# Performance work log

Hardware: AMD Instinct MI355X
Metric: run time of the kernel (lower is better)

Reference implementation:

```python
import jax, jax.numpy as jnp
import numpy as np

TOP_K = 2
N_EXPERTS = 64
NEG_INF = -1e30  # stand-in for -inf; only used implicitly via sparse softmax


def setup_inputs() -> dict:
    key = jax.random.key(0)
    k1, k2, k3, k4 = jax.random.split(key, 4)
    n_embd, n_exp = 2048, N_EXPERTS
    B, S = 4, 4096
    scale = 1.0 / np.sqrt(n_embd)
    return {
        "x": jax.random.normal(k1, (B, S, n_embd), dtype=jnp.float32),
        "noise_eps": jax.random.normal(k2, (B, S, n_exp), dtype=jnp.float32),
        "W_route": jax.random.normal(k3, (n_embd, n_exp), dtype=jnp.float32) * scale,
        "b_route": jnp.zeros((n_exp,), dtype=jnp.float32),
        "W_noise": jax.random.normal(k4, (n_embd, n_exp), dtype=jnp.float32) * scale,
        "b_noise": jnp.zeros((n_exp,), dtype=jnp.float32),
    }


def reference(x, noise_eps, W_route, b_route, W_noise, b_noise):
    # r_act, noise_scale: [B, S, E]
    r_act = jnp.einsum("bsd,de->bse", x, W_route) + b_route
    noise_raw = jnp.einsum("bsd,de->bse", x, W_noise) + b_noise
    noisy = r_act + noise_eps * jax.nn.softplus(noise_raw)

    topk_logits, idx = jax.lax.top_k(noisy, TOP_K)  # [B, S, k]
    # softmax over a -inf-filled scatter == softmax over the top-k values,
    # scattered back with zeros elsewhere (exp(-inf) = 0)
    probs_k = jax.nn.softmax(topk_logits, axis=-1)  # [B, S, k]
    one_hot = jax.nn.one_hot(idx, N_EXPERTS, dtype=probs_k.dtype)  # [B, S, k, E]
    r_out = jnp.einsum("bsk,bske->bse", probs_k, one_hot)
    return r_out, idx
```

## Files before the change

### kernel.cpp

```cpp
#include <hip/hip_runtime.h>
#include <math.h>


typedef _Float16 f16;
typedef _Float16 f16x8 __attribute__((ext_vector_type(8)));
typedef float    f32x4 __attribute__((ext_vector_type(4)));

#define NEMBD 2048
#define NEXP  64
#define TOKB  32
#define PSTR  36
#define PSLC  (128 * PSTR)
#define WSCALE 64.0f
#define INV_WSCALE 0.015625f

union F4H8 { float4 f; f16x8 h; };

__device__ __forceinline__ f16x8 ld16h(const f16* p) {
    F4H8 u; u.f = *(const float4*)p; return u.h;
}

__global__ __launch_bounds__(256) void build_wt(
    const float* __restrict__ Wr, const float* __restrict__ Wn,
    f16* __restrict__ wt_hi, f16* __restrict__ wt_lo)
{
    __shared__ float ws[32][129];
    const int c = blockIdx.x, t = threadIdx.x;
    const int k0 = c * 32;
    {
        const int k  = t >> 3;
        const int n8 = (t & 7) << 3;
        const float* s0 = Wr + (size_t)(k0 + k) * NEXP + n8;
        const float* s1 = Wn + (size_t)(k0 + k) * NEXP + n8;
        #pragma unroll
        for (int j = 0; j < 8; ++j) ws[k][n8 + j] = s0[j];
        #pragma unroll
        for (int j = 0; j < 8; ++j) ws[k][64 + n8 + j] = s1[j];
    }
    __syncthreads();
    {
        const int n  = t >> 1;
        const int kh = (t & 1) << 4;
        f16x8 hv0, hv1, lv0, lv1;
        #pragma unroll
        for (int j = 0; j < 8; ++j) {
            const float v = ws[kh + j][n] * WSCALE;
            const f16 h = (f16)v;
            hv0[j] = h; lv0[j] = (f16)(v - (float)h);
        }
        #pragma unroll
        for (int j = 0; j < 8; ++j) {
            const float v = ws[kh + 8 + j][n] * WSCALE;
            const f16 h = (f16)v;
            hv1[j] = h; lv1[j] = (f16)(v - (float)h);
        }
        const size_t base = ((size_t)c * 128 + n) * 32 + kh;
        *(f16x8*)(wt_hi + base)     = hv0;
        *(f16x8*)(wt_hi + base + 8) = hv1;
        *(f16x8*)(wt_lo + base)     = lv0;
        *(f16x8*)(wt_lo + base + 8) = lv1;
    }
}

__global__ __launch_bounds__(512, 4) void router_fused6(
    const float* __restrict__ x, const float* __restrict__ eps,
    const f16* __restrict__ wt_hi, const f16* __restrict__ wt_lo,
    const float* __restrict__ br, const float* __restrict__ bn,
    float* __restrict__ out_r, float* __restrict__ out_idx)
{
    __shared__ __align__(16) float P[4 * PSLC];
    __shared__ float TK[4 * TOKB];

    const int tid  = threadIdx.x;
    const int lane = tid & 63;
    const int w    = tid >> 6;
    const int m0   = blockIdx.x * TOKB;

    const int row16 = lane & 15;
    const int kgrp  = (lane >> 4) << 3;

    const float* asrc0 = x + (size_t)(m0 + row16) * NEMBD + w * 256 + kgrp;
    const float* asrc1 = asrc0 + (size_t)16 * NEMBD;

    const int bofs = row16 * 32 + kgrp;

    f32x4 acc[2][8];
    #pragma unroll
    for (int i = 0; i < 2; ++i)
        #pragma unroll
        for (int f = 0; f < 8; ++f) acc[i][f] = (f32x4){0.f, 0.f, 0.f, 0.f};

#define SPLIT8(A0, A1, ah, al) do { \
    const float av[8] = {A0.x, A0.y, A0.z, A0.w, A1.x, A1.y, A1.z, A1.w}; \
    _Pragma("unroll") \
    for (int j = 0; j < 8; ++j) { \
        const f16 h = (f16)av[j]; ah[j] = h; al[j] = (f16)(av[j] - (float)h); } \
    } while (0)

    for (int c = 0; c < 8; ++c) {
        const int g = (w << 3) + c;
        const size_t cb = (size_t)g * 4096;
        const f16* bh_base = wt_hi + cb + bofs;
        const f16* bl_base = wt_lo + cb + bofs;

        const float4 a00 = *(const float4*)(asrc0 + c * 32);
        const float4 a01 = *(const float4*)(asrc0 + c * 32 + 4);
        const float4 a10 = *(const float4*)(asrc1 + c * 32);
        const float4 a11 = *(const float4*)(asrc1 + c * 32 + 4);
        f16x8 ah0, al0, ah1, al1;
        SPLIT8(a00, a01, ah0, al0);
        SPLIT8(a10, a11, ah1, al1);

        #pragma unroll
        for (int fg = 0; fg < 4; ++fg) {
            const f16x8 bh0 = ld16h(bh_base + (2 * fg) * 512);
            const f16x8 bl0 = ld16h(bl_base + (2 * fg) * 512);
            const f16x8 bh1 = ld16h(bh_base + (2 * fg + 1) * 512);
            const f16x8 bl1 = ld16h(bl_base + (2 * fg + 1) * 512);
            acc[0][2*fg]   = __builtin_amdgcn_mfma_f32_16x16x32_f16(ah0, bh0, acc[0][2*fg],   0, 0, 0);
            acc[0][2*fg]   = __builtin_amdgcn_mfma_f32_16x16x32_f16(al0, bh0, acc[0][2*fg],   0, 0, 0);
            acc[0][2*fg]   = __builtin_amdgcn_mfma_f32_16x16x32_f16(ah0, bl0, acc[0][2*fg],   0, 0, 0);
            acc[1][2*fg]   = __builtin_amdgcn_mfma_f32_16x16x32_f16(ah1, bh0, acc[1][2*fg],   0, 0, 0);
            acc[1][2*fg]   = __builtin_amdgcn_mfma_f32_16x16x32_f16(al1, bh0, acc[1][2*fg],   0, 0, 0);
            acc[1][2*fg]   = __builtin_amdgcn_mfma_f32_16x16x32_f16(ah1, bl0, acc[1][2*fg],   0, 0, 0);
            acc[0][2*fg+1] = __builtin_amdgcn_mfma_f32_16x16x32_f16(ah0, bh1, acc[0][2*fg+1], 0, 0, 0);
            acc[0][2*fg+1] = __builtin_amdgcn_mfma_f32_16x16x32_f16(al0, bh1, acc[0][2*fg+1], 0, 0, 0);
            acc[0][2*fg+1] = __builtin_amdgcn_mfma_f32_16x16x32_f16(ah0, bl1, acc[0][2*fg+1], 0, 0, 0);
            acc[1][2*fg+1] = __builtin_amdgcn_mfma_f32_16x16x32_f16(ah1, bh1, acc[1][2*fg+1], 0, 0, 0);
            acc[1][2*fg+1] = __builtin_amdgcn_mfma_f32_16x16x32_f16(al1, bh1, acc[1][2*fg+1], 0, 0, 0);
            acc[1][2*fg+1] = __builtin_amdgcn_mfma_f32_16x16x32_f16(ah1, bl1, acc[1][2*fg+1], 0, 0, 0);
        }
    }
#undef SPLIT8

    const int tokb = (lane >> 4) << 2;

    if (w >= 4) {
        float* Pw = P + (w - 4) * PSLC;
        #pragma unroll
        for (int f = 0; f < 8; ++f) {
            const int col = f * 16 + row16;
            #pragma unroll
            for (int i = 0; i < 2; ++i) {
                float4 v;
                v.x = acc[i][f][0] * INV_WSCALE;
                v.y = acc[i][f][1] * INV_WSCALE;
                v.z = acc[i][f][2] * INV_WSCALE;
                v.w = acc[i][f][3] * INV_WSCALE;
                *(float4*)(Pw + col * PSTR + i * 16 + tokb) = v;
            }
        }
    }
    __syncthreads();

    if (w < 4) {
        float* Pw = P + w * PSLC;
        #pragma unroll
        for (int f = 0; f < 8; ++f) {
            const int col = f * 16 + row16;
            #pragma unroll
            for (int i = 0; i < 2; ++i) {
                float* dst = Pw + col * PSTR + i * 16 + tokb;
                float4 d = *(float4*)dst;
                d.x += acc[i][f][0] * INV_WSCALE;
                d.y += acc[i][f][1] * INV_WSCALE;
                d.z += acc[i][f][2] * INV_WSCALE;
                d.w += acc[i][f][3] * INV_WSCALE;
                *(float4*)dst = d;
            }
        }
    }
    __syncthreads();

    #pragma unroll
    for (int k = 0; k < 4; ++k) {
        const int ch  = tid + k * 512;
        const int s   = ch >> 10;
        const int r   = ch & 1023;
        const int col = r >> 3;
        const int tkc = (r & 7) << 2;
        float* dst = P + s * PSLC + col * PSTR + tkc;
        const float* src = P + (s + 2) * PSLC + col * PSTR + tkc;
        float4 d = *(float4*)dst;
        const float4 sv = *(const float4*)src;
        d.x += sv.x; d.y += sv.y; d.z += sv.z; d.w += sv.w;
        *(float4*)dst = d;
    }
    __syncthreads();

    #pragma unroll
    for (int k = 0; k < 2; ++k) {
        const int r   = tid + k * 512;
        const int col = r >> 3;
        const int tkc = (r & 7) << 2;
        float* dst = P + col * PSTR + tkc;
        const float* src = P + PSLC + col * PSTR + tkc;
        float4 d = *(float4*)dst;
        const float4 sv = *(const float4*)src;
        d.x += sv.x; d.y += sv.y; d.z += sv.z; d.w += sv.w;
        *(float4*)dst = d;
    }
    __syncthreads();

    if (tid < 128) {
        const int t = tid >> 2;
        const int q = tid & 3;
        const float* ep = eps + (size_t)(m0 + t) * NEXP;
        float v1 = -1e30f, v2 = -1e30f;
        int i1 = 0, i2 = 0;
        for (int j = 0; j < 16; ++j) {
            const int e = q * 16 + j;
            const float r  = br[e] + P[e * PSTR + t];
            const float nr = bn[e] + P[(NEXP + e) * PSTR + t];
            const float sp = fmaxf(nr, 0.f) + log1pf(expf(-fabsf(nr)));
            const float noisy = fmaf(ep[e], sp, r);
            if (noisy > v1) { v2 = v1; i2 = i1; v1 = noisy; i1 = e; }
            else if (noisy > v2) { v2 = noisy; i2 = e; }
        }
        #pragma unroll
        for (int s = 0; s < 2; ++s) {
            const int dist = 1 << s;
            const float ov1 = __shfl_xor(v1, dist);
            const float ov2 = __shfl_xor(v2, dist);
            const int   oi1 = __shfl_xor(i1, dist);
            const int   oi2 = __shfl_xor(i2, dist);
            const int h = (q >> s) & 1;
            float a1, a2, bb1, bb2; int ai1, ai2, bj1, bj2;
            if (h) { a1 = ov1; a2 = ov2; ai1 = oi1; ai2 = oi2; bb1 = v1;  bb2 = v2;  bj1 = i1;  bj2 = i2; }
            else   { a1 = v1;  a2 = v2;  ai1 = i1;  ai2 = i2;  bb1 = ov1; bb2 = ov2; bj1 = oi1; bj2 = oi2; }
            if (bb1 > a1) {
                v1 = bb1; i1 = bj1;
                if (a1 >= bb2) { v2 = a1; i2 = ai1; } else { v2 = bb2; i2 = bj2; }
            } else {
                v1 = a1; i1 = ai1;
                if (bb1 > a2) { v2 = bb1; i2 = bj1; } else { v2 = a2; i2 = ai2; }
            }
        }
        if (q == 0) {
            const float e2 = expf(v2 - v1);
            const float p1 = 1.f / (1.f + e2);
            TK[0 * TOKB + t] = p1;
            TK[1 * TOKB + t] = e2 * p1;
            TK[2 * TOKB + t] = (float)i1;
            TK[3 * TOKB + t] = (float)i2;
        }
    }
    __syncthreads();

    {
        const int t  = tid >> 4;
        const int c4 = (tid & 15) << 2;
        const float p1 = TK[t], p2 = TK[TOKB + t];
        const int i1 = (int)TK[2 * TOKB + t], i2 = (int)TK[3 * TOKB + t];
        float buf[4];
        #pragma unroll
        for (int jj = 0; jj < 4; ++jj) {
            const int e = c4 + jj;
            buf[jj] = (e == i1) ? p1 : (e == i2) ? p2 : 0.f;
        }
        *(float4*)(out_r + (size_t)(m0 + t) * NEXP + c4) = *(float4*)buf;
    }
    if (tid < TOKB) {
        float2 v = make_float2(TK[2 * TOKB + tid], TK[3 * TOKB + tid]);
        *(float2*)(out_idx + (size_t)(m0 + tid) * 2) = v;
    }
}

__global__ __launch_bounds__(256) void router_fused_f32(
    const float* __restrict__ x, const float* __restrict__ eps,
    const float* __restrict__ Wr, const float* __restrict__ br,
    const float* __restrict__ Wn, const float* __restrict__ bn,
    float* __restrict__ out_r, float* __restrict__ out_idx)
{
    __shared__ float xs[32][64];
    __shared__ float ws2[32][128];
    __shared__ float lg[128][64];
    __shared__ float tk[4][64];
    const int tid = threadIdx.x;
    const int tx = tid & 15, ty = tid >> 4;
    const int m0 = blockIdx.x * 64;
    float acc[4][8];
    #pragma unroll
    for (int i = 0; i < 4; ++i)
        #pragma unroll
        for (int j = 0; j < 8; ++j) acc[i][j] = 0.f;
    for (int kc = 0; kc < NEMBD; kc += 32) {
        {
            const int tm = tid >> 2, kk = (tid & 3) << 3;
            const float* src = x + (size_t)(m0 + tm) * NEMBD + kc + kk;
            const float4 a = *(const float4*)(src);
            const float4 b = *(const float4*)(src + 4);
            xs[kk+0][tm]=a.x; xs[kk+1][tm]=a.y; xs[kk+2][tm]=a.z; xs[kk+3][tm]=a.w;
            xs[kk+4][tm]=b.x; xs[kk+5][tm]=b.y; xs[kk+6][tm]=b.z; xs[kk+7][tm]=b.w;
        }
        {
            const int kr = tid >> 3, q = tid & 7;
            const float* src = (q < 4)
                ? (Wr + (size_t)(kc + kr) * NEXP + (q << 4))
                : (Wn + (size_t)(kc + kr) * NEXP + ((q - 4) << 4));
            float* dst = &ws2[kr][q << 4];
            #pragma unroll
            for (int j = 0; j < 16; ++j) dst[j] = src[j];
        }
        __syncthreads();
        #pragma unroll
        for (int k = 0; k < 32; ++k) {
            const float4 xv = *(const float4*)&xs[k][ty << 2];
            const float4 wa = *(const float4*)&ws2[k][tx << 3];
            const float4 wb = *(const float4*)&ws2[k][(tx << 3) + 4];
            const float xr[4] = {xv.x, xv.y, xv.z, xv.w};
            const float wcx[8] = {wa.x, wa.y, wa.z, wa.w, wb.x, wb.y, wb.z, wb.w};
            #pragma unroll
            for (int i = 0; i < 4; ++i)
                #pragma unroll
                for (int j = 0; j < 8; ++j)
                    acc[i][j] = fmaf(xr[i], wcx[j], acc[i][j]);
        }
        __syncthreads();
    }
    {
        const int n0 = tx << 3;
        #pragma unroll
        for (int j = 0; j < 8; ++j) {
            const int n = n0 + j;
            const float b = (n < NEXP) ? br[n] : bn[n - NEXP];
            #pragma unroll
            for (int i = 0; i < 4; ++i)
                lg[n][(ty << 2) + i] = acc[i][j] + b;
        }
    }
    __syncthreads();
    if (tid < 64) {
        const int t = tid;
        const float* ep = eps + (size_t)(m0 + t) * NEXP;
        float v1 = -1e30f, v2 = -1e30f; int i1 = 0, i2 = 0;
        for (int e = 0; e < NEXP; ++e) {
            const float r = lg[e][t], nr = lg[NEXP + e][t];
            const float sp = fmaxf(nr, 0.f) + log1pf(expf(-fabsf(nr)));
            const float noisy = fmaf(ep[e], sp, r);
            if (noisy > v1) { v2=v1; i2=i1; v1=noisy; i1=e; }
            else if (noisy > v2) { v2=noisy; i2=e; }
        }
        const float e2 = expf(v2 - v1);
        const float p1 = 1.f / (1.f + e2);
        tk[0][t]=p1; tk[1][t]=e2*p1; tk[2][t]=(float)i1; tk[3][t]=(float)i2;
    }
    __syncthreads();
    {
        const int t = tid >> 2, c = tid & 3;
        const float p1 = tk[0][t], p2 = tk[1][t];
        const int i1 = (int)tk[2][t], i2 = (int)tk[3][t];
        float buf[16];
        #pragma unroll
        for (int j = 0; j < 16; ++j) {
            const int e = (c << 4) + j;
            buf[j] = (e == i1) ? p1 : (e == i2) ? p2 : 0.f;
        }
        float* dst = out_r + (size_t)(m0 + t) * NEXP + (c << 4);
        *(float4*)(dst+0)=*(float4*)(buf+0); *(float4*)(dst+4)=*(float4*)(buf+4);
        *(float4*)(dst+8)=*(float4*)(buf+8); *(float4*)(dst+12)=*(float4*)(buf+12);
    }
    if (tid < 64) {
        float2 v = make_float2(tk[2][tid], tk[3][tid]);
        *(float2*)(out_idx + (size_t)(m0 + tid) * 2) = v;
    }
}

extern "C" void kernel_launch(void* const* d_in, const int* in_sizes, int n_in,
                              void* d_out, int out_size, void* d_ws, size_t ws_size,
                              hipStream_t stream) {
    const float* x  = (const float*)d_in[0];
    const float* ep = (const float*)d_in[1];
    const float* Wr = (const float*)d_in[2];
    const float* br = (const float*)d_in[3];
    const float* Wn = (const float*)d_in[4];
    const float* bn = (const float*)d_in[5];

    const int T = in_sizes[1] / NEXP;
    float* out_r   = (float*)d_out;
    float* out_idx = (float*)d_out + (size_t)T * NEXP;

    const size_t limb = (size_t)128 * NEMBD * sizeof(f16);
    if (ws_size >= 2 * limb) {
        f16* wt_hi = (f16*)d_ws;
        f16* wt_lo = wt_hi + (size_t)128 * NEMBD;
        build_wt<<<64, 256, 0, stream>>>(Wr, Wn, wt_hi, wt_lo);
        router_fused6<<<T / TOKB, 512, 0, stream>>>(
            x, ep, wt_hi, wt_lo, br, bn, out_r, out_idx);
    } else {
        router_fused_f32<<<T / 64, 256, 0, stream>>>(
            x, ep, Wr, br, Wn, bn, out_r, out_idx);
    }
}
```

Baseline: 66.04 us.

## Split router GEMM work by output columns and K halves to shrink LDS reduction

Changes the per-wave work split from 8-way K-splitting over all 128 columns to 4 column groups times 2 K halves, so each wave holds only 4 accumulators and walks 32 K chunks. This drops the LDS partial-sum buffer from four slices to one and removes two reduction passes and their barriers. The smaller register and LDS footprint allows launch bounds to request 8 blocks per CU. In exchange, each wave now reloads its x tile for its K half, so the four column-group waves sharing a half all fetch the same x data. Each wave also has a longer serial loop with fewer independent MFMA chains to hide latency.

```diff
diff --git a/kernel.cpp b/kernel.cpp
--- a/kernel.cpp
+++ b/kernel.cpp
@@ -10,7 +10,6 @@
 #define NEXP  64
 #define TOKB  32
 #define PSTR  36
-#define PSLC  (128 * PSTR)
 #define WSCALE 64.0f
 #define INV_WSCALE 0.015625f
 
@@ -62,33 +61,33 @@
     }
 }
 
-__global__ __launch_bounds__(512, 4) void router_fused6(
+__global__ __launch_bounds__(512, 8) void router_fused7(
     const float* __restrict__ x, const float* __restrict__ eps,
     const f16* __restrict__ wt_hi, const f16* __restrict__ wt_lo,
     const float* __restrict__ br, const float* __restrict__ bn,
     float* __restrict__ out_r, float* __restrict__ out_idx)
 {
-    __shared__ __align__(16) float P[4 * PSLC];
+    __shared__ __align__(16) float P[128 * PSTR];
     __shared__ float TK[4 * TOKB];
 
     const int tid  = threadIdx.x;
     const int lane = tid & 63;
     const int w    = tid >> 6;
+    const int cq   = w & 3;
+    const int kh   = w >> 2;
     const int m0   = blockIdx.x * TOKB;
 
     const int row16 = lane & 15;
     const int kgrp  = (lane >> 4) << 3;
 
-    const float* asrc0 = x + (size_t)(m0 + row16) * NEMBD + w * 256 + kgrp;
+    const float* asrc0 = x + (size_t)(m0 + row16) * NEMBD + kh * 1024 + kgrp;
     const float* asrc1 = asrc0 + (size_t)16 * NEMBD;
 
-    const int bofs = row16 * 32 + kgrp;
-
-    f32x4 acc[2][8];
-    #pragma unroll
-    for (int i = 0; i < 2; ++i)
-        #pragma unroll
-        for (int f = 0; f < 8; ++f) acc[i][f] = (f32x4){0.f, 0.f, 0.f, 0.f};
+    const int bofs0 = (cq * 32 + row16) * 32 + kgrp;
+    const int bofs1 = (cq * 32 + 16 + row16) * 32 + kgrp;
+
+    f32x4 acc00 = {0.f,0.f,0.f,0.f}, acc01 = {0.f,0.f,0.f,0.f};
+    f32x4 acc10 = {0.f,0.f,0.f,0.f}, acc11 = {0.f,0.f,0.f,0.f};
 
 #define SPLIT8(A0, A1, ah, al) do { \
     const float av[8] = {A0.x, A0.y, A0.z, A0.w, A1.x, A1.y, A1.z, A1.w}; \
@@ -97,12 +96,8 @@
         const f16 h = (f16)av[j]; ah[j] = h; al[j] = (f16)(av[j] - (float)h); } \
     } while (0)
 
-    for (int c = 0; c < 8; ++c) {
-        const int g = (w << 3) + c;
-        const size_t cb = (size_t)g * 4096;
-        const f16* bh_base = wt_hi + cb + bofs;
-        const f16* bl_base = wt_lo + cb + bofs;
-
+    for (int c = 0; c < 32; ++c) {
+        const size_t cb = (size_t)(kh * 32 + c) * 4096;
         const float4 a00 = *(const float4*)(asrc0 + c * 32);
         const float4 a01 = *(const float4*)(asrc0 + c * 32 + 4);
         const float4 a10 = *(const float4*)(asrc1 + c * 32);
@@ -111,94 +106,61 @@
         SPLIT8(a00, a01, ah0, al0);
         SPLIT8(a10, a11, ah1, al1);
 
-        #pragma unroll
-        for (int fg = 0; fg < 4; ++fg) {
-            const f16x8 bh0 = ld16h(bh_base + (2 * fg) * 512);
-            const f16x8 bl0 = ld16h(bl_base + (2 * fg) * 512);
-            const f16x8 bh1 = ld16h(bh_base + (2 * fg + 1) * 512);
-            const f16x8 bl1 = ld16h(bl_base + (2 * fg + 1) * 512);
-            acc[0][2*fg]   = __builtin_amdgcn_mfma_f32_16x16x32_f16(ah0, bh0, acc[0][2*fg],   0, 0, 0);
-            acc[0][2*fg]   = __builtin_amdgcn_mfma_f32_16x16x32_f16(al0, bh0, acc[0][2*fg],   0, 0, 0);
-            acc[0][2*fg]   = __builtin_amdgcn_mfma_f32_16x16x32_f16(ah0, bl0, acc[0][2*fg],   0, 0, 0);
-            acc[1][2*fg]   = __builtin_amdgcn_mfma_f32_16x16x32_f16(ah1, bh0, acc[1][2*fg],   0, 0, 0);
-            acc[1][2*fg]   = __builtin_amdgcn_mfma_f32_16x16x32_f16(al1, bh0, acc[1][2*fg],   0, 0, 0);
-            acc[1][2*fg]   = __builtin_amdgcn_mfma_f32_16x16x32_f16(ah1, bl0, acc[1][2*fg],   0, 0, 0);
-            acc[0][2*fg+1] = __builtin_amdgcn_mfma_f32_16x16x32_f16(ah0, bh1, acc[0][2*fg+1], 0, 0, 0);
-            acc[0][2*fg+1] = __builtin_amdgcn_mfma_f32_16x16x32_f16(al0, bh1, acc[0][2*fg+1], 0, 0, 0);
-            acc[0][2*fg+1] = __builtin_amdgcn_mfma_f32_16x16x32_f16(ah0, bl1, acc[0][2*fg+1], 0, 0, 0);
-            acc[1][2*fg+1] = __builtin_amdgcn_mfma_f32_16x16x32_f16(ah1, bh1, acc[1][2*fg+1], 0, 0, 0);
-            acc[1][2*fg+1] = __builtin_amdgcn_mfma_f32_16x16x32_f16(al1, bh1, acc[1][2*fg+1], 0, 0, 0);
-            acc[1][2*fg+1] = __builtin_amdgcn_mfma_f32_16x16x32_f16(ah1, bl1, acc[1][2*fg+1], 0, 0, 0);
+        {
+            const f16x8 bh = ld16h(wt_hi + cb + bofs0);
+            const f16x8 bl = ld16h(wt_lo + cb + bofs0);
+            acc00 = __builtin_amdgcn_mfma_f32_16x16x32_f16(ah0, bh, acc00, 0, 0, 0);
+            acc00 = __builtin_amdgcn_mfma_f32_16x16x32_f16(al0, bh, acc00, 0, 0, 0);
+            acc00 = __builtin_amdgcn_mfma_f32_16x16x32_f16(ah0, bl, acc00, 0, 0, 0);
+            acc10 = __builtin_amdgcn_mfma_f32_16x16x32_f16(ah1, bh, acc10, 0, 0, 0);
+            acc10 = __builtin_amdgcn_mfma_f32_16x16x32_f16(al1, bh, acc10, 0, 0, 0);
+            acc10 = __builtin_amdgcn_mfma_f32_16x16x32_f16(ah1, bl, acc10, 0, 0, 0);
+        }
+        {
+            const f16x8 bh = ld16h(wt_hi + cb + bofs1);
+            const f16x8 bl = ld16h(wt_lo + cb + bofs1);
+            acc01 = __builtin_amdgcn_mfma_f32_16x16x32_f16(ah0, bh, acc01, 0, 0, 0);
+            acc01 = __builtin_amdgcn_mfma_f32_16x16x32_f16(al0, bh, acc01, 0, 0, 0);
+            acc01 = __builtin_amdgcn_mfma_f32_16x16x32_f16(ah0, bl, acc01, 0, 0, 0);
+            acc11 = __builtin_amdgcn_mfma_f32_16x16x32_f16(ah1, bh, acc11, 0, 0, 0);
+            acc11 = __builtin_amdgcn_mfma_f32_16x16x32_f16(al1, bh, acc11, 0, 0, 0);
+            acc11 = __builtin_amdgcn_mfma_f32_16x16x32_f16(ah1, bl, acc11, 0, 0, 0);
         }
     }
 #undef SPLIT8
 
     const int tokb = (lane >> 4) << 2;
-
-    if (w >= 4) {
-        float* Pw = P + (w - 4) * PSLC;
-        #pragma unroll
-        for (int f = 0; f < 8; ++f) {
-            const int col = f * 16 + row16;
-            #pragma unroll
-            for (int i = 0; i < 2; ++i) {
+    if (kh == 1) {
+        #pragma unroll
+        for (int i = 0; i < 2; ++i) {
+            #pragma unroll
+            for (int j = 0; j < 2; ++j) {
+                const f32x4 a = (i == 0) ? (j == 0 ? acc00 : acc01)
+                                         : (j == 0 ? acc10 : acc11);
+                const int col = cq * 32 + j * 16 + row16;
                 float4 v;
-                v.x = acc[i][f][0] * INV_WSCALE;
-                v.y = acc[i][f][1] * INV_WSCALE;
-                v.z = acc[i][f][2] * INV_WSCALE;
-                v.w = acc[i][f][3] * INV_WSCALE;
-                *(float4*)(Pw + col * PSTR + i * 16 + tokb) = v;
+                v.x = a[0] * INV_WSCALE; v.y = a[1] * INV_WSCALE;
+                v.z = a[2] * INV_WSCALE; v.w = a[3] * INV_WSCALE;
+                *(float4*)(P + col * PSTR + i * 16 + tokb) = v;
             }
         }
     }
     __syncthreads();
-
-    if (w < 4) {
-        float* Pw = P + w * PSLC;
-        #pragma unroll
-        for (int f = 0; f < 8; ++f) {
-            const int col = f * 16 + row16;
-            #pragma unroll
-            for (int i = 0; i < 2; ++i) {
-                float* dst = Pw + col * PSTR + i * 16 + tokb;
+    if (kh == 0) {
+        #pragma unroll
+        for (int i = 0; i < 2; ++i) {
+            #pragma unroll
+            for (int j = 0; j < 2; ++j) {
+                const f32x4 a = (i == 0) ? (j == 0 ? acc00 : acc01)
+                                         : (j == 0 ? acc10 : acc11);
+                const int col = cq * 32 + j * 16 + row16;
+                float* dst = P + col * PSTR + i * 16 + tokb;
                 float4 d = *(float4*)dst;
-                d.x += acc[i][f][0] * INV_WSCALE;
-                d.y += acc[i][f][1] * INV_WSCALE;
-                d.z += acc[i][f][2] * INV_WSCALE;
-                d.w += acc[i][f][3] * INV_WSCALE;
+                d.x += a[0] * INV_WSCALE; d.y += a[1] * INV_WSCALE;
+                d.z += a[2] * INV_WSCALE; d.w += a[3] * INV_WSCALE;
                 *(float4*)dst = d;
             }
         }
-    }
-    __syncthreads();
-
-    #pragma unroll
-    for (int k = 0; k < 4; ++k) {
-        const int ch  = tid + k * 512;
-        const int s   = ch >> 10;
-        const int r   = ch & 1023;
-        const int col = r >> 3;
-        const int tkc = (r & 7) << 2;
-        float* dst = P + s * PSLC + col * PSTR + tkc;
-        const float* src = P + (s + 2) * PSLC + col * PSTR + tkc;
-        float4 d = *(float4*)dst;
-        const float4 sv = *(const float4*)src;
-        d.x += sv.x; d.y += sv.y; d.z += sv.z; d.w += sv.w;
-        *(float4*)dst = d;
-    }
-    __syncthreads();
-
-    #pragma unroll
-    for (int k = 0; k < 2; ++k) {
-        const int r   = tid + k * 512;
-        const int col = r >> 3;
-        const int tkc = (r & 7) << 2;
-        float* dst = P + col * PSTR + tkc;
-        const float* src = P + PSLC + col * PSTR + tkc;
-        float4 d = *(float4*)dst;
-        const float4 sv = *(const float4*)src;
-        d.x += sv.x; d.y += sv.y; d.z += sv.z; d.w += sv.w;
-        *(float4*)dst = d;
     }
     __syncthreads();
 
@@ -385,7 +347,7 @@
         f16* wt_hi = (f16*)d_ws;
         f16* wt_lo = wt_hi + (size_t)128 * NEMBD;
         build_wt<<<64, 256, 0, stream>>>(Wr, Wn, wt_hi, wt_lo);
-        router_fused6<<<T / TOKB, 512, 0, stream>>>(
+        router_fused7<<<T / TOKB, 512, 0, stream>>>(
             x, ep, wt_hi, wt_lo, br, bn, out_r, out_idx);
     } else {
         router_fused_f32<<<T / 64, 256, 0, stream>>>(
```

Result: slower. 104.9 us (+58.9%).
